# Kernel optimization log

Hardware: AMD Instinct MI355X
Metric: run time of the kernel (lower is better)

## Reference

```python
import jax, jax.numpy as jnp
import numpy as np

B, CIN, COUT, H, W = 64, 2048, 32, 14, 14
REP = 1024


def setup_inputs() -> dict:
    key = jax.random.key(0)
    ks = jax.random.split(key, 7)
    x = jax.random.normal(ks[0], (B, CIN, H, W), dtype=jnp.float32)
    conv_w = jax.random.normal(ks[1], (COUT, CIN, 3, 3), dtype=jnp.float32) * (1.0 / np.sqrt(CIN * 9))
    conv_b = jax.random.normal(ks[2], (COUT,), dtype=jnp.float32) * 0.01
    w6 = jax.random.normal(ks[3], (REP, CIN * COUT), dtype=jnp.float32) * (1.0 / np.sqrt(CIN * COUT))
    b6 = jax.random.normal(ks[4], (REP,), dtype=jnp.float32) * 0.01
    w7 = jax.random.normal(ks[5], (REP, REP), dtype=jnp.float32) * (1.0 / np.sqrt(REP))
    b7 = jax.random.normal(ks[6], (REP,), dtype=jnp.float32) * 0.01
    return {"x": x, "conv_w": conv_w, "conv_b": conv_b,
            "w6": w6, "b6": b6, "w7": w7, "b7": b7}


def reference(x, conv_w, conv_b, w6, b6, w7, b7):
    # attention_map = Conv2d(in->out, k=3, s=1, p=1)(x)  -> [B, COUT, H, W]
    am = jax.lax.conv_general_dilated(
        x, conv_w, window_strides=(1, 1), padding=((1, 1), (1, 1)),
        dimension_numbers=("NCHW", "OIHW", "NCHW"))
    am = am + conv_b[None, :, None, None]
    # outer product am[:,None]*x[:,:,None] followed by AdaptiveAvgPool2d(1)
    # == mean over HW of the product: [B, CIN, COUT]
    hw = x.shape[2] * x.shape[3]
    pooled = jnp.einsum("bihw,bohw->bio", x, am) / hw
    feat = pooled.reshape(pooled.shape[0], -1)          # [B, CIN*COUT]
    h6 = jax.nn.relu(feat @ w6.T + b6)                  # [B, REP]
    out = jax.nn.relu(h6 @ w7.T + b7)                   # [B, REP]
    return out
```

## Files before the change

### kernel.cpp

```cpp
#include <hip/hip_runtime.h>
#include <hip/hip_bf16.h>

#define B_   64
#define CIN  2048
#define COUT 32
#define P    196
#define PPAD 224
#define REP  1024
#define K1   (CIN*COUT)

typedef float  f32x4  __attribute__((ext_vector_type(4)));
typedef __bf16 bf16x8 __attribute__((ext_vector_type(8)));
typedef __bf16 bf16x4 __attribute__((ext_vector_type(4)));

#define OFF_AM     0
#define OFF_H6PRE  (OFF_AM + B_*COUT*PPAD*4)
#define OFF_H7PRE  (OFF_H6PRE + B_*REP*4)
#define ZERO_BYTES (OFF_H7PRE + B_*REP*4)
#define OFF_POOLED ((size_t)ZERO_BYTES)
#define OFF_H6B    (OFF_POOLED + (size_t)B_*K1*2)

__global__ __launch_bounds__(256)
void conv_kernel(const float* __restrict__ x, const float* __restrict__ cw,
                 float* __restrict__ am) {
  __shared__ __bf16 XT[256][32];
  __shared__ __bf16 WL[9][32][32];

  const int b     = blockIdx.y;
  const int chunk = blockIdx.x;
  const int t     = threadIdx.x;
  const int wv    = t >> 6;
  const int lane  = t & 63;
  const int q     = lane >> 4;
  const int ln    = lane & 15;
  const int ot    = wv >> 1;
  const int w0    = wv & 1;

  f32x4 acc[7];
  #pragma unroll
  for (int i = 0; i < 7; i++) { f32x4 z = {0.f,0.f,0.f,0.f}; acc[i] = z; }

  const float* xb = x + (size_t)b * CIN * P;

  for (int s = 0; s < 8; s++) {
    const int i0 = chunk * 256 + s * 32;
    __syncthreads();
    unsigned int* xz = (unsigned int*)&XT[0][0];
    #pragma unroll
    for (int idx = t; idx < 4096; idx += 256) xz[idx] = 0u;
    __syncthreads();
    for (int idx = t; idx < 32 * P; idx += 256) {
      int il = idx / P;
      int p  = idx - il * P;
      float v = xb[(size_t)(i0 + il) * P + p];
      int h = p / 14, w = p - h * 14;
      XT[(h + 1) * 16 + (w + 1)][il] = (__bf16)v;
    }
    for (int idx = t; idx < 9216; idx += 256) {
      int o  = idx / 288;
      int r  = idx - o * 288;
      int il = r / 9;
      int d  = r - il * 9;
      float v = cw[(size_t)o * (CIN * 9) + (size_t)(i0 + il) * 9 + d];
      WL[d][o][il] = (__bf16)v;
    }
    __syncthreads();

    bf16x8 af[9];
    #pragma unroll
    for (int d = 0; d < 9; d++)
      af[d] = *(const bf16x8*)&WL[d][ot * 16 + ln][q * 8];

    #pragma unroll
    for (int pi = 0; pi < 7; pi++) {
      int pt = w0 + 2 * pi;
      if (pt > 12) break;
      int p  = pt * 16 + ln;
      int pp = p < P ? p : P - 1;
      int h  = pp / 14, w = pp - (pp / 14) * 14;
      #pragma unroll
      for (int d = 0; d < 9; d++) {
        int dy = d / 3, dx = d - (d / 3) * 3;
        bf16x8 bfr = *(const bf16x8*)&XT[(h + dy) * 16 + (w + dx)][q * 8];
        acc[pi] = __builtin_amdgcn_mfma_f32_16x16x32_bf16(af[d], bfr, acc[pi], 0, 0, 0);
      }
    }
  }

  #pragma unroll
  for (int pi = 0; pi < 7; pi++) {
    int pt = w0 + 2 * pi;
    if (pt > 12) break;
    int p = pt * 16 + ln;
    if (p < P) {
      #pragma unroll
      for (int r = 0; r < 4; r++) {
        int o = ot * 16 + q * 4 + r;
        atomicAdd(&am[((size_t)b * COUT + o) * PPAD + p], acc[pi][r]);
      }
    }
  }
}

__global__ __launch_bounds__(256)
void pooled_kernel(const float* __restrict__ x, const float* __restrict__ amp,
                   const float* __restrict__ cb, __bf16* __restrict__ pooled) {
  const int b    = blockIdx.y;
  const int ig   = blockIdx.x;
  const int t    = threadIdx.x;
  const int wv   = t >> 6;
  const int lane = t & 63;
  const int q    = lane >> 4;
  const int ln   = lane & 15;
  const int ibase = ig * 256 + wv * 64;

  f32x4 acc[2][4];
  #pragma unroll
  for (int a = 0; a < 2; a++)
    #pragma unroll
    for (int c = 0; c < 4; c++) { f32x4 z = {0.f,0.f,0.f,0.f}; acc[a][c] = z; }

  const float* amb = amp + (size_t)b * COUT * PPAD;
  const float* xb  = x + (size_t)b * CIN * P;
  const float cbv[2] = { cb[ln], cb[16 + ln] };

  for (int kc = 0; kc < 7; kc++) {
    const int k0 = kc * 32;
    bf16x8 af[2];
    if (kc < 6) {
      #pragma unroll
      for (int o2 = 0; o2 < 2; o2++) {
        const float* src = &amb[(size_t)(o2 * 16 + ln) * PPAD + k0 + q * 8];
        f32x4 v0 = *(const f32x4*)src;
        f32x4 v1 = *(const f32x4*)(src + 4);
        bf16x8 a;
        #pragma unroll
        for (int j = 0; j < 4; j++) { a[j] = (__bf16)(v0[j] + cbv[o2]); a[4 + j] = (__bf16)(v1[j] + cbv[o2]); }
        af[o2] = a;
      }
    } else {
      #pragma unroll
      for (int o2 = 0; o2 < 2; o2++) {
        bf16x8 a;
        #pragma unroll
        for (int j = 0; j < 8; j++) {
          int p = k0 + q * 8 + j;
          a[j] = (p < P) ? (__bf16)(amb[(size_t)(o2 * 16 + ln) * PPAD + p] + cbv[o2]) : (__bf16)0.f;
        }
        af[o2] = a;
      }
    }
    #pragma unroll
    for (int it = 0; it < 4; it++) {
      const int i = ibase + it * 16 + ln;
      bf16x8 bfr;
      if (kc < 6) {
        const float* src = &xb[(size_t)i * P + k0 + q * 8];
        f32x4 v0 = *(const f32x4*)src;
        f32x4 v1 = *(const f32x4*)(src + 4);
        #pragma unroll
        for (int j = 0; j < 4; j++) { bfr[j] = (__bf16)v0[j]; bfr[4 + j] = (__bf16)v1[j]; }
      } else {
        #pragma unroll
        for (int j = 0; j < 8; j++) {
          int p = k0 + q * 8 + j;
          bfr[j] = (p < P) ? (__bf16)xb[(size_t)i * P + p] : (__bf16)0.f;
        }
      }
      acc[0][it] = __builtin_amdgcn_mfma_f32_16x16x32_bf16(af[0], bfr, acc[0][it], 0, 0, 0);
      acc[1][it] = __builtin_amdgcn_mfma_f32_16x16x32_bf16(af[1], bfr, acc[1][it], 0, 0, 0);
    }
  }

  const float sc = 1.0f / 196.0f;
  #pragma unroll
  for (int o2 = 0; o2 < 2; o2++)
    #pragma unroll
    for (int it = 0; it < 4; it++) {
      const int i = ibase + it * 16 + ln;
      bf16x4 vv;
      #pragma unroll
      for (int r = 0; r < 4; r++) vv[r] = (__bf16)(acc[o2][it][r] * sc);
      *(bf16x4*)&pooled[(size_t)b * K1 + (size_t)i * COUT + o2 * 16 + q * 4] = vv;
    }
}

__global__ __launch_bounds__(256)
void gemm1_kernel(const __bf16* __restrict__ pooled, const float* __restrict__ w6,
                  float* __restrict__ h6pre) {
  const int nb   = blockIdx.x;
  const int ks   = blockIdx.y;
  const int t    = threadIdx.x;
  const int wv   = t >> 6;
  const int lane = t & 63;
  const int q    = lane >> 4;
  const int ln   = lane & 15;
  const int n0   = nb * 256 + wv * 64;

  f32x4 acc[4][4];
  #pragma unroll
  for (int a = 0; a < 4; a++)
    #pragma unroll
    for (int c = 0; c < 4; c++) { f32x4 z = {0.f,0.f,0.f,0.f}; acc[a][c] = z; }

  for (int kc = 0; kc < 32; kc++) {
    const int k0 = ks * 1024 + kc * 32;
    bf16x8 af[4];
    #pragma unroll
    for (int mi = 0; mi < 4; mi++)
      af[mi] = *(const bf16x8*)&pooled[(size_t)(mi * 16 + ln) * K1 + k0 + q * 8];
    #pragma unroll
    for (int ni = 0; ni < 4; ni++) {
      const float* src = &w6[(size_t)(n0 + ni * 16 + ln) * K1 + k0 + q * 8];
      f32x4 v0 = *(const f32x4*)src;
      f32x4 v1 = *(const f32x4*)(src + 4);
      bf16x8 bfr;
      #pragma unroll
      for (int j = 0; j < 4; j++) { bfr[j] = (__bf16)v0[j]; bfr[4 + j] = (__bf16)v1[j]; }
      #pragma unroll
      for (int mi = 0; mi < 4; mi++)
        acc[mi][ni] = __builtin_amdgcn_mfma_f32_16x16x32_bf16(af[mi], bfr, acc[mi][ni], 0, 0, 0);
    }
  }
  #pragma unroll
  for (int mi = 0; mi < 4; mi++)
    #pragma unroll
    for (int ni = 0; ni < 4; ni++)
      #pragma unroll
      for (int r = 0; r < 4; r++) {
        int bb = mi * 16 + q * 4 + r;
        int rr = n0 + ni * 16 + ln;
        atomicAdd(&h6pre[(size_t)bb * REP + rr], acc[mi][ni][r]);
      }
}

__global__ void h6act_kernel(const float* __restrict__ h6pre, const float* __restrict__ b6,
                             __bf16* __restrict__ h6b) {
  int idx = blockIdx.x * 256 + threadIdx.x;
  float v = h6pre[idx] + b6[idx & (REP - 1)];
  h6b[idx] = (__bf16)fmaxf(v, 0.f);
}

__global__ __launch_bounds__(256)
void gemm2_kernel(const __bf16* __restrict__ h6b, const float* __restrict__ w7,
                  float* __restrict__ h7pre) {
  const int nb   = blockIdx.x;
  const int ks   = blockIdx.y;
  const int t    = threadIdx.x;
  const int wv   = t >> 6;
  const int lane = t & 63;
  const int q    = lane >> 4;
  const int ln   = lane & 15;
  const int n0   = nb * 64 + wv * 16;

  f32x4 acc[4];
  #pragma unroll
  for (int a = 0; a < 4; a++) { f32x4 z = {0.f,0.f,0.f,0.f}; acc[a] = z; }

  #pragma unroll
  for (int kc = 0; kc < 2; kc++) {
    const int k0 = ks * 64 + kc * 32;
    const float* src = &w7[(size_t)(n0 + ln) * REP + k0 + q * 8];
    f32x4 v0 = *(const f32x4*)src;
    f32x4 v1 = *(const f32x4*)(src + 4);
    bf16x8 bfr;
    #pragma unroll
    for (int j = 0; j < 4; j++) { bfr[j] = (__bf16)v0[j]; bfr[4 + j] = (__bf16)v1[j]; }
    #pragma unroll
    for (int mi = 0; mi < 4; mi++) {
      bf16x8 af = *(const bf16x8*)&h6b[(size_t)(mi * 16 + ln) * REP + k0 + q * 8];
      acc[mi] = __builtin_amdgcn_mfma_f32_16x16x32_bf16(af, bfr, acc[mi], 0, 0, 0);
    }
  }
  #pragma unroll
  for (int mi = 0; mi < 4; mi++)
    #pragma unroll
    for (int r = 0; r < 4; r++) {
      int bb = mi * 16 + q * 4 + r;
      atomicAdd(&h7pre[(size_t)bb * REP + n0 + ln], acc[mi][r]);
    }
}

__global__ void outact_kernel(const float* __restrict__ h7pre, const float* __restrict__ b7,
                              float* __restrict__ out) {
  int idx = blockIdx.x * 256 + threadIdx.x;
  float v = h7pre[idx] + b7[idx & (REP - 1)];
  out[idx] = fmaxf(v, 0.f);
}

extern "C" void kernel_launch(void* const* d_in, const int* in_sizes, int n_in,
                              void* d_out, int out_size, void* d_ws, size_t ws_size,
                              hipStream_t stream) {
  const float* x   = (const float*)d_in[0];
  const float* cw  = (const float*)d_in[1];
  const float* cb  = (const float*)d_in[2];
  const float* w6  = (const float*)d_in[3];
  const float* b6  = (const float*)d_in[4];
  const float* w7  = (const float*)d_in[5];
  const float* b7  = (const float*)d_in[6];
  float* out = (float*)d_out;

  char* ws = (char*)d_ws;
  float*  am     = (float*)(ws + OFF_AM);
  float*  h6pre  = (float*)(ws + OFF_H6PRE);
  float*  h7pre  = (float*)(ws + OFF_H7PRE);
  __bf16* pooled = (__bf16*)(ws + OFF_POOLED);
  __bf16* h6b    = (__bf16*)(ws + OFF_H6B);

  hipMemsetAsync(ws, 0, ZERO_BYTES, stream);

  conv_kernel  <<<dim3(8, 64),  256, 0, stream>>>(x, cw, am);
  pooled_kernel<<<dim3(8, 64),  256, 0, stream>>>(x, am, cb, pooled);
  gemm1_kernel <<<dim3(4, 64),  256, 0, stream>>>(pooled, w6, h6pre);
  h6act_kernel <<<256,          256, 0, stream>>>(h6pre, b6, h6b);
  gemm2_kernel <<<dim3(16, 16), 256, 0, stream>>>(h6b, w7, h7pre);
  outact_kernel<<<256,          256, 0, stream>>>(h7pre, b7, out);
}
```

Before: 632.0 us.

## Recast conv as per-tap GEMMs plus shift-combine and replace atomics with split-K reductions

```diff
diff --git a/kernel.cpp b/kernel.cpp
--- a/kernel.cpp
+++ b/kernel.cpp
@@ -13,149 +13,159 @@
 typedef __bf16 bf16x8 __attribute__((ext_vector_type(8)));
 typedef __bf16 bf16x4 __attribute__((ext_vector_type(4)));
 
-#define OFF_AM     0
-#define OFF_H6PRE  (OFF_AM + B_*COUT*PPAD*4)
-#define OFF_H7PRE  (OFF_H6PRE + B_*REP*4)
-#define ZERO_BYTES (OFF_H7PRE + B_*REP*4)
-#define OFF_POOLED ((size_t)ZERO_BYTES)
-#define OFF_H6B    (OFF_POOLED + (size_t)B_*K1*2)
-
-__global__ __launch_bounds__(256)
-void conv_kernel(const float* __restrict__ x, const float* __restrict__ cw,
-                 float* __restrict__ am) {
-  __shared__ __bf16 XT[256][32];
-  __shared__ __bf16 WL[9][32][32];
-
-  const int b     = blockIdx.y;
-  const int chunk = blockIdx.x;
-  const int t     = threadIdx.x;
-  const int wv    = t >> 6;
-  const int lane  = t & 63;
-  const int q     = lane >> 4;
-  const int ln    = lane & 15;
-  const int ot    = wv >> 1;
-  const int w0    = wv & 1;
-
-  f32x4 acc[7];
-  #pragma unroll
-  for (int i = 0; i < 7; i++) { f32x4 z = {0.f,0.f,0.f,0.f}; acc[i] = z; }
-
-  const float* xb = x + (size_t)b * CIN * P;
-
-  for (int s = 0; s < 8; s++) {
-    const int i0 = chunk * 256 + s * 32;
-    __syncthreads();
-    unsigned int* xz = (unsigned int*)&XT[0][0];
-    #pragma unroll
-    for (int idx = t; idx < 4096; idx += 256) xz[idx] = 0u;
-    __syncthreads();
-    for (int idx = t; idx < 32 * P; idx += 256) {
-      int il = idx / P;
-      int p  = idx - il * P;
-      float v = xb[(size_t)(i0 + il) * P + p];
-      int h = p / 14, w = p - h * 14;
-      XT[(h + 1) * 16 + (w + 1)][il] = (__bf16)v;
-    }
-    for (int idx = t; idx < 9216; idx += 256) {
-      int o  = idx / 288;
-      int r  = idx - o * 288;
-      int il = r / 9;
-      int d  = r - il * 9;
-      float v = cw[(size_t)o * (CIN * 9) + (size_t)(i0 + il) * 9 + d];
-      WL[d][o][il] = (__bf16)v;
-    }
-    __syncthreads();
-
-    bf16x8 af[9];
-    #pragma unroll
-    for (int d = 0; d < 9; d++)
-      af[d] = *(const bf16x8*)&WL[d][ot * 16 + ln][q * 8];
-
-    #pragma unroll
-    for (int pi = 0; pi < 7; pi++) {
-      int pt = w0 + 2 * pi;
-      if (pt > 12) break;
-      int p  = pt * 16 + ln;
-      int pp = p < P ? p : P - 1;
-      int h  = pp / 14, w = pp - (pp / 14) * 14;
-      #pragma unroll
-      for (int d = 0; d < 9; d++) {
-        int dy = d / 3, dx = d - (d / 3) * 3;
-        bf16x8 bfr = *(const bf16x8*)&XT[(h + dy) * 16 + (w + dx)][q * 8];
-        acc[pi] = __builtin_amdgcn_mfma_f32_16x16x32_bf16(af[d], bfr, acc[pi], 0, 0, 0);
+#define OFF_R1     0
+#define OFF_R2     16777216
+#define OFF_W2     25165824
+#define OFF_AM     26345472
+#define OFF_H6B    28180480
+
+static __device__ __forceinline__ f32x4 mfma16(bf16x8 a, bf16x8 b, f32x4 c) {
+  return __builtin_amdgcn_mfma_f32_16x16x32_bf16(a, b, c, 0, 0, 0);
+}
+
+__global__ __launch_bounds__(256)
+void prep_w2(const float* __restrict__ cw, __bf16* __restrict__ W2) {
+  const int blk = blockIdx.x;
+  const int o = blk >> 3, cc = blk & 7;
+  const int cin = cc * 256 + threadIdx.x;
+  const float* src = cw + ((size_t)o * CIN + cin) * 9;
+  #pragma unroll
+  for (int d = 0; d < 9; d++)
+    W2[((size_t)d * COUT + o) * CIN + cin] = (__bf16)src[d];
+}
+
+__global__ __launch_bounds__(576)
+void sgemm_kernel(const float* __restrict__ x, const __bf16* __restrict__ W2,
+                  float* __restrict__ S) {
+  const int nb = blockIdx.x;
+  const int b  = blockIdx.y;
+  const int d  = threadIdx.x >> 6;
+  const int lane = threadIdx.x & 63;
+  const int q = lane >> 4, ln = lane & 15;
+  const int n0 = nb * 32;
+  const int p0 = n0 + ln, p1 = n0 + 16 + ln;
+
+  const __bf16* A  = W2 + (size_t)d * COUT * CIN;
+  const float*  xb = x + (size_t)b * CIN * P;
+
+  f32x4 acc[2][2];
+  #pragma unroll
+  for (int m = 0; m < 2; m++)
+    #pragma unroll
+    for (int n = 0; n < 2; n++) { f32x4 z = {0.f,0.f,0.f,0.f}; acc[m][n] = z; }
+
+  if (nb < 6) {
+    #pragma unroll 2
+    for (int kc = 0; kc < 64; kc++) {
+      const int k0 = kc * 32 + q * 8;
+      bf16x8 a0 = *(const bf16x8*)&A[(size_t)ln * CIN + k0];
+      bf16x8 a1 = *(const bf16x8*)&A[(size_t)(16 + ln) * CIN + k0];
+      bf16x8 b0, b1;
+      const float* xk = xb + (size_t)k0 * P;
+      #pragma unroll
+      for (int j = 0; j < 8; j++) {
+        b0[j] = (__bf16)xk[(size_t)j * P + p0];
+        b1[j] = (__bf16)xk[(size_t)j * P + p1];
       }
-    }
-  }
-
-  #pragma unroll
-  for (int pi = 0; pi < 7; pi++) {
-    int pt = w0 + 2 * pi;
-    if (pt > 12) break;
-    int p = pt * 16 + ln;
+      acc[0][0] = mfma16(a0, b0, acc[0][0]);
+      acc[0][1] = mfma16(a0, b1, acc[0][1]);
+      acc[1][0] = mfma16(a1, b0, acc[1][0]);
+      acc[1][1] = mfma16(a1, b1, acc[1][1]);
+    }
+  } else {
+    #pragma unroll 2
+    for (int kc = 0; kc < 64; kc++) {
+      const int k0 = kc * 32 + q * 8;
+      bf16x8 a0 = *(const bf16x8*)&A[(size_t)ln * CIN + k0];
+      bf16x8 a1 = *(const bf16x8*)&A[(size_t)(16 + ln) * CIN + k0];
+      bf16x8 b0, b1;
+      const float* xk = xb + (size_t)k0 * P;
+      #pragma unroll
+      for (int j = 0; j < 8; j++) {
+        b0[j] = (p0 < P) ? (__bf16)xk[(size_t)j * P + p0] : (__bf16)0.f;
+        b1[j] = (__bf16)0.f;
+      }
+      acc[0][0] = mfma16(a0, b0, acc[0][0]);
+      acc[0][1] = mfma16(a0, b1, acc[0][1]);
+      acc[1][0] = mfma16(a1, b0, acc[1][0]);
+      acc[1][1] = mfma16(a1, b1, acc[1][1]);
+    }
+  }
+
+  #pragma unroll
+  for (int mt = 0; mt < 2; mt++)
+    #pragma unroll
+    for (int nt = 0; nt < 2; nt++) {
+      const int p = n0 + nt * 16 + ln;
+      float* dst = &S[(((size_t)b * 9 + d) * COUT + mt * 16 + q * 4) * PPAD + p];
+      #pragma unroll
+      for (int r = 0; r < 4; r++) dst[(size_t)r * PPAD] = acc[mt][nt][r];
+    }
+}
+
+__global__ __launch_bounds__(256)
+void combine_kernel(const float* __restrict__ S, float* __restrict__ am) {
+  const int b = blockIdx.x >> 2, part = blockIdx.x & 3;
+  const float* Sb = S + (size_t)b * 9 * COUT * PPAD;
+  for (int i = threadIdx.x; i < 1792; i += 256) {
+    const int idx = part * 1792 + i;
+    const int o = idx / PPAD, p = idx - o * PPAD;
+    float s = 0.f;
     if (p < P) {
-      #pragma unroll
-      for (int r = 0; r < 4; r++) {
-        int o = ot * 16 + q * 4 + r;
-        atomicAdd(&am[((size_t)b * COUT + o) * PPAD + p], acc[pi][r]);
-      }
-    }
+      const int h = p / 14, w = p - (p / 14) * 14;
+      #pragma unroll
+      for (int dy = 0; dy < 3; dy++)
+        #pragma unroll
+        for (int dx = 0; dx < 3; dx++) {
+          const int hh = h + dy - 1, ww = w + dx - 1;
+          if (hh >= 0 && hh < 14 && ww >= 0 && ww < 14)
+            s += Sb[((size_t)(dy * 3 + dx) * COUT + o) * PPAD + hh * 14 + ww];
+        }
+    }
+    am[((size_t)b * COUT + o) * PPAD + p] = s;
   }
 }
 
 __global__ __launch_bounds__(256)
 void pooled_kernel(const float* __restrict__ x, const float* __restrict__ amp,
                    const float* __restrict__ cb, __bf16* __restrict__ pooled) {
-  const int b    = blockIdx.y;
-  const int ig   = blockIdx.x;
-  const int t    = threadIdx.x;
-  const int wv   = t >> 6;
+  const int b  = blockIdx.y;
+  const int ig = blockIdx.x;
+  const int t  = threadIdx.x;
+  const int wv = t >> 6;
   const int lane = t & 63;
-  const int q    = lane >> 4;
-  const int ln   = lane & 15;
-  const int ibase = ig * 256 + wv * 64;
-
-  f32x4 acc[2][4];
+  const int q = lane >> 4, ln = lane & 15;
+  const int ibase = ig * 128 + wv * 32;
+
+  f32x4 acc[2][2];
   #pragma unroll
   for (int a = 0; a < 2; a++)
     #pragma unroll
-    for (int c = 0; c < 4; c++) { f32x4 z = {0.f,0.f,0.f,0.f}; acc[a][c] = z; }
+    for (int c = 0; c < 2; c++) { f32x4 z = {0.f,0.f,0.f,0.f}; acc[a][c] = z; }
 
   const float* amb = amp + (size_t)b * COUT * PPAD;
   const float* xb  = x + (size_t)b * CIN * P;
   const float cbv[2] = { cb[ln], cb[16 + ln] };
 
   for (int kc = 0; kc < 7; kc++) {
-    const int k0 = kc * 32;
+    const int k0 = kc * 32 + q * 8;
     bf16x8 af[2];
-    if (kc < 6) {
-      #pragma unroll
-      for (int o2 = 0; o2 < 2; o2++) {
-        const float* src = &amb[(size_t)(o2 * 16 + ln) * PPAD + k0 + q * 8];
-        f32x4 v0 = *(const f32x4*)src;
-        f32x4 v1 = *(const f32x4*)(src + 4);
-        bf16x8 a;
-        #pragma unroll
-        for (int j = 0; j < 4; j++) { a[j] = (__bf16)(v0[j] + cbv[o2]); a[4 + j] = (__bf16)(v1[j] + cbv[o2]); }
-        af[o2] = a;
-      }
-    } else {
-      #pragma unroll
-      for (int o2 = 0; o2 < 2; o2++) {
-        bf16x8 a;
-        #pragma unroll
-        for (int j = 0; j < 8; j++) {
-          int p = k0 + q * 8 + j;
-          a[j] = (p < P) ? (__bf16)(amb[(size_t)(o2 * 16 + ln) * PPAD + p] + cbv[o2]) : (__bf16)0.f;
-        }
-        af[o2] = a;
-      }
-    }
-    #pragma unroll
-    for (int it = 0; it < 4; it++) {
+    #pragma unroll
+    for (int o2 = 0; o2 < 2; o2++) {
+      const float* src = &amb[(size_t)(o2 * 16 + ln) * PPAD + k0];
+      f32x4 v0 = *(const f32x4*)src;
+      f32x4 v1 = *(const f32x4*)(src + 4);
+      bf16x8 a;
+      #pragma unroll
+      for (int j = 0; j < 4; j++) { a[j] = (__bf16)(v0[j] + cbv[o2]); a[4 + j] = (__bf16)(v1[j] + cbv[o2]); }
+      af[o2] = a;
+    }
+    #pragma unroll
+    for (int it = 0; it < 2; it++) {
       const int i = ibase + it * 16 + ln;
       bf16x8 bfr;
       if (kc < 6) {
-        const float* src = &xb[(size_t)i * P + k0 + q * 8];
+        const float* src = &xb[(size_t)i * P + k0];
         f32x4 v0 = *(const f32x4*)src;
         f32x4 v1 = *(const f32x4*)(src + 4);
         #pragma unroll
@@ -163,12 +173,12 @@
       } else {
         #pragma unroll
         for (int j = 0; j < 8; j++) {
-          int p = k0 + q * 8 + j;
+          const int p = k0 + j;
           bfr[j] = (p < P) ? (__bf16)xb[(size_t)i * P + p] : (__bf16)0.f;
         }
       }
-      acc[0][it] = __builtin_amdgcn_mfma_f32_16x16x32_bf16(af[0], bfr, acc[0][it], 0, 0, 0);
-      acc[1][it] = __builtin_amdgcn_mfma_f32_16x16x32_bf16(af[1], bfr, acc[1][it], 0, 0, 0);
+      acc[0][it] = mfma16(af[0], bfr, acc[0][it]);
+      acc[1][it] = mfma16(af[1], bfr, acc[1][it]);
     }
   }
 
@@ -176,7 +186,7 @@
   #pragma unroll
   for (int o2 = 0; o2 < 2; o2++)
     #pragma unroll
-    for (int it = 0; it < 4; it++) {
+    for (int it = 0; it < 2; it++) {
       const int i = ibase + it * 16 + ln;
       bf16x4 vv;
       #pragma unroll
@@ -187,80 +197,23 @@
 
 __global__ __launch_bounds__(256)
 void gemm1_kernel(const __bf16* __restrict__ pooled, const float* __restrict__ w6,
-                  float* __restrict__ h6pre) {
-  const int nb   = blockIdx.x;
-  const int ks   = blockIdx.y;
-  const int t    = threadIdx.x;
-  const int wv   = t >> 6;
+                  float* __restrict__ S1) {
+  const int nb = blockIdx.x, ks = blockIdx.y;
+  const int t = threadIdx.x;
+  const int wv = t >> 6;
   const int lane = t & 63;
-  const int q    = lane >> 4;
-  const int ln   = lane & 15;
-  const int n0   = nb * 256 + wv * 64;
-
-  f32x4 acc[4][4];
-  #pragma unroll
-  for (int a = 0; a < 4; a++)
-    #pragma unroll
-    for (int c = 0; c < 4; c++) { f32x4 z = {0.f,0.f,0.f,0.f}; acc[a][c] = z; }
-
+  const int q = lane >> 4, ln = lane & 15;
+  const int n0 = nb * 64 + wv * 16;
+  const int kbase = ks * 1024;
+
+  f32x4 acc[4];
+  #pragma unroll
+  for (int a = 0; a < 4; a++) { f32x4 z = {0.f,0.f,0.f,0.f}; acc[a] = z; }
+
+  #pragma unroll 2
   for (int kc = 0; kc < 32; kc++) {
-    const int k0 = ks * 1024 + kc * 32;
-    bf16x8 af[4];
-    #pragma unroll
-    for (int mi = 0; mi < 4; mi++)
-      af[mi] = *(const bf16x8*)&pooled[(size_t)(mi * 16 + ln) * K1 + k0 + q * 8];
-    #pragma unroll
-    for (int ni = 0; ni < 4; ni++) {
-      const float* src = &w6[(size_t)(n0 + ni * 16 + ln) * K1 + k0 + q * 8];
-      f32x4 v0 = *(const f32x4*)src;
-      f32x4 v1 = *(const f32x4*)(src + 4);
-      bf16x8 bfr;
-      #pragma unroll
-      for (int j = 0; j < 4; j++) { bfr[j] = (__bf16)v0[j]; bfr[4 + j] = (__bf16)v1[j]; }
-      #pragma unroll
-      for (int mi = 0; mi < 4; mi++)
-        acc[mi][ni] = __builtin_amdgcn_mfma_f32_16x16x32_bf16(af[mi], bfr, acc[mi][ni], 0, 0, 0);
-    }
-  }
-  #pragma unroll
-  for (int mi = 0; mi < 4; mi++)
-    #pragma unroll
-    for (int ni = 0; ni < 4; ni++)
-      #pragma unroll
-      for (int r = 0; r < 4; r++) {
-        int bb = mi * 16 + q * 4 + r;
-        int rr = n0 + ni * 16 + ln;
-        atomicAdd(&h6pre[(size_t)bb * REP + rr], acc[mi][ni][r]);
-      }
-}
-
-__global__ void h6act_kernel(const float* __restrict__ h6pre, const float* __restrict__ b6,
-                             __bf16* __restrict__ h6b) {
-  int idx = blockIdx.x * 256 + threadIdx.x;
-  float v = h6pre[idx] + b6[idx & (REP - 1)];
-  h6b[idx] = (__bf16)fmaxf(v, 0.f);
-}
-
-__global__ __launch_bounds__(256)
-void gemm2_kernel(const __bf16* __restrict__ h6b, const float* __restrict__ w7,
-                  float* __restrict__ h7pre) {
-  const int nb   = blockIdx.x;
-  const int ks   = blockIdx.y;
-  const int t    = threadIdx.x;
-  const int wv   = t >> 6;
-  const int lane = t & 63;
-  const int q    = lane >> 4;
-  const int ln   = lane & 15;
-  const int n0   = nb * 64 + wv * 16;
-
-  f32x4 acc[4];
-  #pragma unroll
-  for (int a = 0; a < 4; a++) { f32x4 z = {0.f,0.f,0.f,0.f}; acc[a] = z; }
-
-  #pragma unroll
-  for (int kc = 0; kc < 2; kc++) {
-    const int k0 = ks * 64 + kc * 32;
-    const float* src = &w7[(size_t)(n0 + ln) * REP + k0 + q * 8];
+    const int k0 = kbase + kc * 32 + q * 8;
+    const float* src = &w6[(size_t)(n0 + ln) * K1 + k0];
     f32x4 v0 = *(const f32x4*)src;
     f32x4 v1 = *(const f32x4*)(src + 4);
     bf16x8 bfr;
@@ -268,24 +221,67 @@
     for (int j = 0; j < 4; j++) { bfr[j] = (__bf16)v0[j]; bfr[4 + j] = (__bf16)v1[j]; }
     #pragma unroll
     for (int mi = 0; mi < 4; mi++) {
-      bf16x8 af = *(const bf16x8*)&h6b[(size_t)(mi * 16 + ln) * REP + k0 + q * 8];
-      acc[mi] = __builtin_amdgcn_mfma_f32_16x16x32_bf16(af, bfr, acc[mi], 0, 0, 0);
+      bf16x8 af = *(const bf16x8*)&pooled[(size_t)(mi * 16 + ln) * K1 + k0];
+      acc[mi] = mfma16(af, bfr, acc[mi]);
     }
   }
   #pragma unroll
   for (int mi = 0; mi < 4; mi++)
     #pragma unroll
-    for (int r = 0; r < 4; r++) {
-      int bb = mi * 16 + q * 4 + r;
-      atomicAdd(&h7pre[(size_t)bb * REP + n0 + ln], acc[mi][r]);
-    }
-}
-
-__global__ void outact_kernel(const float* __restrict__ h7pre, const float* __restrict__ b7,
-                              float* __restrict__ out) {
-  int idx = blockIdx.x * 256 + threadIdx.x;
-  float v = h7pre[idx] + b7[idx & (REP - 1)];
-  out[idx] = fmaxf(v, 0.f);
+    for (int r = 0; r < 4; r++)
+      S1[(size_t)ks * (B_ * REP) + (size_t)(mi * 16 + q * 4 + r) * REP + n0 + ln] = acc[mi][r];
+}
+
+__global__ __launch_bounds__(256)
+void reduce1_kernel(const float* __restrict__ S1, const float* __restrict__ b6,
+                    __bf16* __restrict__ h6b) {
+  const int idx = blockIdx.x * 256 + threadIdx.x;
+  float s = 0.f;
+  #pragma unroll 8
+  for (int ks = 0; ks < 64; ks++) s += S1[(size_t)ks * (B_ * REP) + idx];
+  h6b[idx] = (__bf16)fmaxf(s + b6[idx & (REP - 1)], 0.f);
+}
+
+__global__ __launch_bounds__(256)
+void gemm2_kernel(const __bf16* __restrict__ h6b, const float* __restrict__ w7,
+                  float* __restrict__ S2) {
+  const int nb = blockIdx.x, ks = blockIdx.y;
+  const int t = threadIdx.x;
+  const int wv = t >> 6;
+  const int lane = t & 63;
+  const int q = lane >> 4, ln = lane & 15;
+  const int n0 = nb * 64 + wv * 16;
+  const int k0 = ks * 32 + q * 8;
+
+  const float* src = &w7[(size_t)(n0 + ln) * REP + k0];
+  f32x4 v0 = *(const f32x4*)src;
+  f32x4 v1 = *(const f32x4*)(src + 4);
+  bf16x8 bfr;
+  #pragma unroll
+  for (int j = 0; j < 4; j++) { bfr[j] = (__bf16)v0[j]; bfr[4 + j] = (__bf16)v1[j]; }
+
+  f32x4 acc[4];
+  #pragma unroll
+  for (int mi = 0; mi < 4; mi++) {
+    f32x4 z = {0.f,0.f,0.f,0.f};
+    bf16x8 af = *(const bf16x8*)&h6b[(size_t)(mi * 16 + ln) * REP + k0];
+    acc[mi] = mfma16(af, bfr, z);
+  }
+  #pragma unroll
+  for (int mi = 0; mi < 4; mi++)
+    #pragma unroll
+    for (int r = 0; r < 4; r++)
+      S2[(size_t)ks * (B_ * REP) + (size_t)(mi * 16 + q * 4 + r) * REP + n0 + ln] = acc[mi][r];
+}
+
+__global__ __launch_bounds__(256)
+void reduce2_kernel(const float* __restrict__ S2, const float* __restrict__ b7,
+                    float* __restrict__ out) {
+  const int idx = blockIdx.x * 256 + threadIdx.x;
+  float s = 0.f;
+  #pragma unroll 8
+  for (int ks = 0; ks < 32; ks++) s += S2[(size_t)ks * (B_ * REP) + idx];
+  out[idx] = fmaxf(s + b7[idx & (REP - 1)], 0.f);
 }
 
 extern "C" void kernel_launch(void* const* d_in, const int* in_sizes, int n_in,
@@ -301,18 +297,20 @@
   float* out = (float*)d_out;
 
   char* ws = (char*)d_ws;
+  float*  S      = (float*)(ws + OFF_R1);
+  float*  S1     = (float*)(ws + OFF_R1);
+  __bf16* pooled = (__bf16*)(ws + OFF_R2);
+  float*  S2     = (float*)(ws + OFF_R2);
+  __bf16* W2     = (__bf16*)(ws + OFF_W2);
   float*  am     = (float*)(ws + OFF_AM);
-  float*  h6pre  = (float*)(ws + OFF_H6PRE);
-  float*  h7pre  = (float*)(ws + OFF_H7PRE);
-  __bf16* pooled = (__bf16*)(ws + OFF_POOLED);
   __bf16* h6b    = (__bf16*)(ws + OFF_H6B);
 
-  hipMemsetAsync(ws, 0, ZERO_BYTES, stream);
-
-  conv_kernel  <<<dim3(8, 64),  256, 0, stream>>>(x, cw, am);
-  pooled_kernel<<<dim3(8, 64),  256, 0, stream>>>(x, am, cb, pooled);
-  gemm1_kernel <<<dim3(4, 64),  256, 0, stream>>>(pooled, w6, h6pre);
-  h6act_kernel <<<256,          256, 0, stream>>>(h6pre, b6, h6b);
-  gemm2_kernel <<<dim3(16, 16), 256, 0, stream>>>(h6b, w7, h7pre);
-  outact_kernel<<<256,          256, 0, stream>>>(h7pre, b7, out);
-}
+  prep_w2       <<<256,          256, 0, stream>>>(cw, W2);
+  sgemm_kernel  <<<dim3(7, 64),  576, 0, stream>>>(x, W2, S);
+  combine_kernel<<<256,          256, 0, stream>>>(S, am);
+  pooled_kernel <<<dim3(16, 64), 256, 0, stream>>>(x, am, cb, pooled);
+  gemm1_kernel  <<<dim3(16, 64), 256, 0, stream>>>(pooled, w6, S1);
+  reduce1_kernel<<<256,          256, 0, stream>>>(S1, b6, h6b);
+  gemm2_kernel  <<<dim3(16, 32), 256, 0, stream>>>(h6b, w7, S2);
+  reduce2_kernel<<<256,          256, 0, stream>>>(S2, b7, out);
+}
```

New measurement: 722.6 us. +14.3%, slower.
